# Optimization experiments

Measured on AMD Instinct MI355X. Metric: run time of the kernel, lower is better.

Reference implementation:

```python
import jax, jax.numpy as jnp
import numpy as np

N, E = 50000, 800000
IN_DIM, HID, OUT_DIM = 512, 64, 40


def setup_inputs() -> dict:
    key = jax.random.key(0)
    ks = jax.random.split(key, 7)
    X = jax.random.normal(ks[0], (N, IN_DIM), dtype=jnp.float32)
    edges = jax.random.randint(ks[1], (2, E), 0, N, dtype=jnp.int64)
    # GCNConv weight (glorot) and bias
    W1 = jax.random.normal(ks[2], (IN_DIM, HID), dtype=jnp.float32) / np.sqrt(IN_DIM)
    b1 = jnp.zeros((HID,), dtype=jnp.float32)
    # fc Linear
    Wfc = jax.random.normal(ks[3], (OUT_DIM, HID), dtype=jnp.float32) / np.sqrt(HID)
    bfc = jax.random.normal(ks[4], (OUT_DIM,), dtype=jnp.float32) * 0.01
    return {"X": X, "edges": edges, "W1": W1, "b1": b1, "Wfc": Wfc, "bfc": bfc}


def gcn_conv(x, src, dst, W, b, n):
    # PyG GCNConv: transform, add self-loops, symmetric D^-1/2 A D^-1/2 norm,
    # scatter-add messages at destination, add bias.
    h = x @ W  # [N, HID]
    loop = jnp.arange(n, dtype=src.dtype)
    src = jnp.concatenate([src, loop])
    dst = jnp.concatenate([dst, loop])
    deg = jax.ops.segment_sum(jnp.ones_like(dst, dtype=h.dtype), dst, num_segments=n)
    dinv = jnp.where(deg > 0, jax.lax.rsqrt(deg), 0.0)
    coef = dinv[src] * dinv[dst]  # [E+N]
    msgs = coef[:, None] * h[src]  # gather + scale
    agg = jax.ops.segment_sum(msgs, dst, num_segments=n)  # scatter-add
    return agg + b


def reference(X, edges, W1, b1, Wfc, bfc):
    n = X.shape[0]
    src, dst = edges[0], edges[1]
    h = jax.nn.relu(gcn_conv(X, src, dst, W1, b1, n))  # [N, HID]
    return h @ Wfc.T + bfc  # [N, OUT_DIM]
```

## Files before the change

### kernel.cpp

```cpp
#include <hip/hip_runtime.h>
#include <hip/hip_bf16.h>

typedef unsigned short u16;
typedef __bf16 bf16_8 __attribute__((ext_vector_type(8)));
typedef float f32_4 __attribute__((ext_vector_type(4)));

#define IN_DIM 512
#define HID 64
#define OUT_DIM 40
#define CAP 64
#define CF_BLOCKS 512

__global__ void k_prep(const float* __restrict__ W1, u16* __restrict__ W1t,
                       int* __restrict__ cnt, int n) {
    int i = blockIdx.x * 256 + threadIdx.x;
    if (i < n) cnt[i] = 0;
    if (i < IN_DIM * HID) {
        int k = i / HID, o = i % HID;
        __hip_bfloat16 v = __float2bfloat16(W1[i]);
        W1t[o * IN_DIM + k] = *reinterpret_cast<u16*>(&v);
    }
}

__launch_bounds__(256)
__global__ void k_work(const float* __restrict__ X, const u16* __restrict__ W1t,
                       const int* __restrict__ src, const int* __restrict__ dst,
                       int* cnt, u16* __restrict__ csr, u16* __restrict__ hs,
                       int N, int E, int NT) {
    __shared__ __align__(16) u16 As[2][64 * 40];
    const int t = threadIdx.x;

    if ((int)blockIdx.x >= NT) {
        int tid = ((int)blockIdx.x - NT) * 256 + t;
        int stride = CF_BLOCKS * 256;
        for (int e = tid; e < E; e += stride) {
            int d = dst[e];
            int p = atomicAdd(&cnt[d], 1);
            if (p < CAP) csr[(size_t)d * CAP + p] = (u16)src[e];
        }
        return;
    }

    const int wave = t >> 6;
    const int lane = t & 63;
    const int m = lane & 15;
    const int quad = lane >> 4;
    const int n0 = blockIdx.x * 64;

    f32_4 acc[4];
    #pragma unroll
    for (int c = 0; c < 4; c++) acc[c] = (f32_4){0.f, 0.f, 0.f, 0.f};

    const int r_st = t >> 2;
    const int k_st = (t & 3) * 8;

    int row = n0 + r_st; if (row >= N) row = N - 1;
    const float* xp = X + (size_t)row * IN_DIM + k_st;

    f32_4 x0 = *reinterpret_cast<const f32_4*>(xp);
    f32_4 x1 = *reinterpret_cast<const f32_4*>(xp + 4);

    int buf = 0;
    for (int k0 = 0; k0 < IN_DIM; k0 += 32) {
        u16 xb[8];
        #pragma unroll
        for (int q = 0; q < 4; q++) {
            __hip_bfloat16 c0 = __float2bfloat16(x0[q]);
            __hip_bfloat16 c1 = __float2bfloat16(x1[q]);
            xb[q]     = *reinterpret_cast<u16*>(&c0);
            xb[4 + q] = *reinterpret_cast<u16*>(&c1);
        }
        *reinterpret_cast<uint4*>(&As[buf][r_st * 40 + k_st]) = *reinterpret_cast<uint4*>(xb);
        __syncthreads();

        if (k0 + 32 < IN_DIM) {
            x0 = *reinterpret_cast<const f32_4*>(xp + k0 + 32);
            x1 = *reinterpret_cast<const f32_4*>(xp + k0 + 36);
        }

        bf16_8 a = *reinterpret_cast<const bf16_8*>(&As[buf][(wave * 16 + m) * 40 + quad * 8]);
        #pragma unroll
        for (int c = 0; c < 4; c++) {
            bf16_8 b = *reinterpret_cast<const bf16_8*>(
                W1t + (size_t)(c * 16 + m) * IN_DIM + k0 + quad * 8);
            acc[c] = __builtin_amdgcn_mfma_f32_16x16x32_bf16(a, b, acc[c], 0, 0, 0);
        }
        buf ^= 1;
    }

    const int nbase = n0 + wave * 16 + quad * 4;
    #pragma unroll
    for (int r = 0; r < 4; r++) {
        int n = nbase + r;
        if (n < N) {
            #pragma unroll
            for (int c = 0; c < 4; c++) {
                __hip_bfloat16 hv = __float2bfloat16(acc[c][r]);
                hs[(size_t)n * HID + c * 16 + m] = *reinterpret_cast<u16*>(&hv);
            }
        }
    }
}

__global__ void k_scale(u16* __restrict__ hs, const int* __restrict__ cnt, int N) {
    int i = blockIdx.x * 256 + threadIdx.x;
    int node = i >> 3;
    if (node >= N) return;
    float dv = rsqrtf((float)cnt[node] + 1.0f);
    uint4 v = *reinterpret_cast<uint4*>(hs + (size_t)i * 8);
    uint vv[4] = {v.x, v.y, v.z, v.w};
    u16 o[8];
    #pragma unroll
    for (int q = 0; q < 4; q++) {
        float lo = __uint_as_float(vv[q] << 16) * dv;
        float hi = __uint_as_float(vv[q] & 0xFFFF0000u) * dv;
        __hip_bfloat16 bl_ = __float2bfloat16(lo);
        __hip_bfloat16 bh_ = __float2bfloat16(hi);
        o[2 * q]     = *reinterpret_cast<u16*>(&bl_);
        o[2 * q + 1] = *reinterpret_cast<u16*>(&bh_);
    }
    *reinterpret_cast<uint4*>(hs + (size_t)i * 8) = *reinterpret_cast<uint4*>(o);
}

__device__ __forceinline__ void acc_add(f32_4& a, uint2 v) {
    a[0] += __uint_as_float(v.x << 16);
    a[1] += __uint_as_float(v.x & 0xFFFF0000u);
    a[2] += __uint_as_float(v.y << 16);
    a[3] += __uint_as_float(v.y & 0xFFFF0000u);
}

#define SHP 72

__launch_bounds__(256)
__global__ void k_aggfc(const u16* __restrict__ hs, const u16* __restrict__ csr,
                        const int* __restrict__ cnt, const float* __restrict__ b1,
                        const float* __restrict__ Wfc, const float* __restrict__ bfc,
                        float* __restrict__ out, int N) {
    __shared__ __align__(16) u16 shb[16 * SHP];
    __shared__ __align__(16) u16 wfb[48 * SHP];
    __shared__ float bl[48];
    const int t = threadIdx.x;

    for (int i = t; i < 48 * HID; i += 256) {
        int o = i / HID, k = i % HID;
        float v = (o < OUT_DIM) ? Wfc[o * HID + k] : 0.f;
        __hip_bfloat16 b = __float2bfloat16(v);
        wfb[o * SHP + k] = *reinterpret_cast<u16*>(&b);
    }
    if (t < 48) bl[t] = (t < OUT_DIM) ? bfc[t] : 0.f;

    const int g = t >> 4, l = t & 15;
    const int n = blockIdx.x * 16 + g;

    if (n < N) {
        const uint2* hs2 = reinterpret_cast<const uint2*>(hs);
        f32_4 a0 = (f32_4){0.f, 0.f, 0.f, 0.f};
        f32_4 a1 = a0, a2 = a0, a3 = a0;
        const float dvn = rsqrtf((float)cnt[n] + 1.0f);
        acc_add(a0, hs2[(size_t)n * 16 + l]);
        int deg = cnt[n]; if (deg > CAP) deg = CAP;
        uint2 cv = reinterpret_cast<const uint2*>(csr + (size_t)n * CAP)[l];
        int j = 0;
        for (; j + 7 < deg; j += 8) {
            int base = j >> 2;
            uint w0x = __shfl(cv.x, base, 16);
            uint w0y = __shfl(cv.y, base, 16);
            uint w1x = __shfl(cv.x, base + 1, 16);
            uint w1y = __shfl(cv.y, base + 1, 16);
            int s0 = (int)(w0x & 0xffff), s1 = (int)(w0x >> 16);
            int s2 = (int)(w0y & 0xffff), s3 = (int)(w0y >> 16);
            int s4 = (int)(w1x & 0xffff), s5 = (int)(w1x >> 16);
            int s6 = (int)(w1y & 0xffff), s7 = (int)(w1y >> 16);
            uint2 v0 = hs2[(size_t)s0 * 16 + l];
            uint2 v1 = hs2[(size_t)s1 * 16 + l];
            uint2 v2 = hs2[(size_t)s2 * 16 + l];
            uint2 v3 = hs2[(size_t)s3 * 16 + l];
            uint2 v4 = hs2[(size_t)s4 * 16 + l];
            uint2 v5 = hs2[(size_t)s5 * 16 + l];
            uint2 v6 = hs2[(size_t)s6 * 16 + l];
            uint2 v7 = hs2[(size_t)s7 * 16 + l];
            acc_add(a0, v0); acc_add(a1, v1);
            acc_add(a2, v2); acc_add(a3, v3);
            acc_add(a0, v4); acc_add(a1, v5);
            acc_add(a2, v6); acc_add(a3, v7);
        }
        for (; j < deg; j++) {
            uint w = __shfl(((j >> 1) & 1) ? cv.y : cv.x, j >> 2, 16);
            int s = (int)((w >> ((j & 1) * 16)) & 0xffff);
            acc_add(a0, hs2[(size_t)s * 16 + l]);
        }
        f32_4 acc = (a0 + a1) + (a2 + a3);
        u16 rb[4];
        #pragma unroll
        for (int q = 0; q < 4; q++) {
            float x = dvn * acc[q] + b1[l * 4 + q];
            x = x > 0.f ? x : 0.f;
            __hip_bfloat16 hb = __float2bfloat16(x);
            rb[q] = *reinterpret_cast<u16*>(&hb);
        }
        *reinterpret_cast<uint2*>(&shb[g * SHP + l * 4]) = *reinterpret_cast<uint2*>(rb);
    }
    __syncthreads();

    const int wave = t >> 6;
    const int lane = t & 63;
    const int m = lane & 15;
    const int quad = lane >> 4;
    if (wave < 3) {
        bf16_8 a0 = *reinterpret_cast<const bf16_8*>(&shb[m * SHP + quad * 8]);
        bf16_8 a1 = *reinterpret_cast<const bf16_8*>(&shb[m * SHP + 32 + quad * 8]);
        bf16_8 b0 = *reinterpret_cast<const bf16_8*>(&wfb[(wave * 16 + m) * SHP + quad * 8]);
        bf16_8 b1 = *reinterpret_cast<const bf16_8*>(&wfb[(wave * 16 + m) * SHP + 32 + quad * 8]);
        f32_4 c = (f32_4){0.f, 0.f, 0.f, 0.f};
        c = __builtin_amdgcn_mfma_f32_16x16x32_bf16(a0, b0, c, 0, 0, 0);
        c = __builtin_amdgcn_mfma_f32_16x16x32_bf16(a1, b1, c, 0, 0, 0);
        const int o = wave * 16 + m;
        if (o < OUT_DIM) {
            const int base = blockIdx.x * 16;
            #pragma unroll
            for (int r = 0; r < 4; r++) {
                int node = base + quad * 4 + r;
                if (node < N) out[(size_t)node * OUT_DIM + o] = c[r] + bl[o];
            }
        }
    }
}


extern "C" void kernel_launch(void* const* d_in, const int* in_sizes, int n_in,
                              void* d_out, int out_size, void* d_ws, size_t ws_size,
                              hipStream_t stream) {
    const float* X   = (const float*)d_in[0];
    const int* edges = (const int*)d_in[1];
    const float* W1  = (const float*)d_in[2];
    const float* b1  = (const float*)d_in[3];
    const float* Wfc = (const float*)d_in[4];
    const float* bfc = (const float*)d_in[5];

    const int N = in_sizes[0] / IN_DIM;
    const int E = in_sizes[1] / 2;
    const int* src = edges;
    const int* dst = edges + E;

    char* p = (char*)d_ws;
    auto carve = [&](size_t bytes) -> char* {
        char* r = p;
        p += (bytes + 255) & ~(size_t)255;
        return r;
    };
    u16* W1t = (u16*)carve((size_t)IN_DIM * HID * 2);
    u16* hs  = (u16*)carve((size_t)N * HID * 2);
    int* cnt = (int*)carve((size_t)N * 4);
    u16* csr = (u16*)carve((size_t)N * CAP * 2);

    const int nb = (N + 255) / 256;
    const int NT = (N + 63) / 64;

    k_prep <<<nb, 256, 0, stream>>>(W1, W1t, cnt, N);
    k_work <<<NT + CF_BLOCKS, 256, 0, stream>>>(X, W1t, src, dst, cnt, csr, hs, N, E, NT);
    k_scale<<<(N * 8 + 255) / 256, 256, 0, stream>>>(hs, cnt, N);
    k_aggfc<<<(N + 15) / 16, 256, 0, stream>>>(hs, csr, cnt, b1, Wfc, bfc,
                                               (float*)d_out, N);
}
```

Baseline: 232.1 us.

## Partition CSR build by destination slice and widen gather loop to 16 neighbors

The CSR fill blocks are now grouped into eight destination-range slices. Each block scans a strided share of the edges, unrolled four at a time, and only does atomics for destinations in its own slice, which is meant to localize atomic and csr write traffic. Every edge is now read by eight blocks, which multiplies dst reads. The aggregation loop now issues 16 neighbor gathers per iteration with clamped indices and masked accumulation, replacing the 8-wide loop plus scalar tail. This raises memory-level parallelism but wastes loads on padded slots.

```diff
diff --git a/kernel.cpp b/kernel.cpp
--- a/kernel.cpp
+++ b/kernel.cpp
@@ -31,12 +31,40 @@
     const int t = threadIdx.x;
 
     if ((int)blockIdx.x >= NT) {
-        int tid = ((int)blockIdx.x - NT) * 256 + t;
-        int stride = CF_BLOCKS * 256;
-        for (int e = tid; e < E; e += stride) {
+        const int slice = (int)blockIdx.x & 7;
+        const int rank  = ((int)blockIdx.x - NT) >> 3;
+        const int lo = (int)(((long)slice * N) >> 3);
+        const int hi = (int)(((long)(slice + 1) * N) >> 3);
+        const int stride = 64 * 256;
+        int e = rank * 256 + t;
+        for (; e + 3 * stride < E; e += 4 * stride) {
+            int d0 = dst[e];
+            int d1 = dst[e + stride];
+            int d2 = dst[e + 2 * stride];
+            int d3 = dst[e + 3 * stride];
+            if (d0 >= lo && d0 < hi) {
+                int p = atomicAdd(&cnt[d0], 1);
+                if (p < CAP) csr[(size_t)d0 * CAP + p] = (u16)src[e];
+            }
+            if (d1 >= lo && d1 < hi) {
+                int p = atomicAdd(&cnt[d1], 1);
+                if (p < CAP) csr[(size_t)d1 * CAP + p] = (u16)src[e + stride];
+            }
+            if (d2 >= lo && d2 < hi) {
+                int p = atomicAdd(&cnt[d2], 1);
+                if (p < CAP) csr[(size_t)d2 * CAP + p] = (u16)src[e + 2 * stride];
+            }
+            if (d3 >= lo && d3 < hi) {
+                int p = atomicAdd(&cnt[d3], 1);
+                if (p < CAP) csr[(size_t)d3 * CAP + p] = (u16)src[e + 3 * stride];
+            }
+        }
+        for (; e < E; e += stride) {
             int d = dst[e];
-            int p = atomicAdd(&cnt[d], 1);
-            if (p < CAP) csr[(size_t)d * CAP + p] = (u16)src[e];
+            if (d >= lo && d < hi) {
+                int p = atomicAdd(&cnt[d], 1);
+                if (p < CAP) csr[(size_t)d * CAP + p] = (u16)src[e];
+            }
         }
         return;
     }
@@ -154,42 +182,43 @@
 
     if (n < N) {
         const uint2* hs2 = reinterpret_cast<const uint2*>(hs);
-        f32_4 a0 = (f32_4){0.f, 0.f, 0.f, 0.f};
-        f32_4 a1 = a0, a2 = a0, a3 = a0;
+        f32_4 aa[4];
+        #pragma unroll
+        for (int q = 0; q < 4; q++) aa[q] = (f32_4){0.f, 0.f, 0.f, 0.f};
         const float dvn = rsqrtf((float)cnt[n] + 1.0f);
-        acc_add(a0, hs2[(size_t)n * 16 + l]);
+        acc_add(aa[0], hs2[(size_t)n * 16 + l]);
         int deg = cnt[n]; if (deg > CAP) deg = CAP;
         uint2 cv = reinterpret_cast<const uint2*>(csr + (size_t)n * CAP)[l];
-        int j = 0;
-        for (; j + 7 < deg; j += 8) {
+        const int nn1 = N - 1;
+        for (int j = 0; j < deg; j += 16) {
             int base = j >> 2;
-            uint w0x = __shfl(cv.x, base, 16);
-            uint w0y = __shfl(cv.y, base, 16);
-            uint w1x = __shfl(cv.x, base + 1, 16);
-            uint w1y = __shfl(cv.y, base + 1, 16);
-            int s0 = (int)(w0x & 0xffff), s1 = (int)(w0x >> 16);
-            int s2 = (int)(w0y & 0xffff), s3 = (int)(w0y >> 16);
-            int s4 = (int)(w1x & 0xffff), s5 = (int)(w1x >> 16);
-            int s6 = (int)(w1y & 0xffff), s7 = (int)(w1y >> 16);
-            uint2 v0 = hs2[(size_t)s0 * 16 + l];
-            uint2 v1 = hs2[(size_t)s1 * 16 + l];
-            uint2 v2 = hs2[(size_t)s2 * 16 + l];
-            uint2 v3 = hs2[(size_t)s3 * 16 + l];
-            uint2 v4 = hs2[(size_t)s4 * 16 + l];
-            uint2 v5 = hs2[(size_t)s5 * 16 + l];
-            uint2 v6 = hs2[(size_t)s6 * 16 + l];
-            uint2 v7 = hs2[(size_t)s7 * 16 + l];
-            acc_add(a0, v0); acc_add(a1, v1);
-            acc_add(a2, v2); acc_add(a3, v3);
-            acc_add(a0, v4); acc_add(a1, v5);
-            acc_add(a2, v6); acc_add(a3, v7);
-        }
-        for (; j < deg; j++) {
-            uint w = __shfl(((j >> 1) & 1) ? cv.y : cv.x, j >> 2, 16);
-            int s = (int)((w >> ((j & 1) * 16)) & 0xffff);
-            acc_add(a0, hs2[(size_t)s * 16 + l]);
-        }
-        f32_4 acc = (a0 + a1) + (a2 + a3);
+            uint wx[4], wy[4];
+            #pragma unroll
+            for (int q = 0; q < 4; q++) {
+                wx[q] = __shfl(cv.x, base + q, 16);
+                wy[q] = __shfl(cv.y, base + q, 16);
+            }
+            int s[16];
+            #pragma unroll
+            for (int q = 0; q < 4; q++) {
+                s[4 * q + 0] = (int)(wx[q] & 0xffff);
+                s[4 * q + 1] = (int)(wx[q] >> 16);
+                s[4 * q + 2] = (int)(wy[q] & 0xffff);
+                s[4 * q + 3] = (int)(wy[q] >> 16);
+            }
+            uint2 v[16];
+            #pragma unroll
+            for (int i = 0; i < 16; i++) {
+                int si = s[i] < nn1 ? s[i] : nn1;
+                v[i] = hs2[(size_t)si * 16 + l];
+            }
+            #pragma unroll
+            for (int i = 0; i < 16; i++) {
+                if (j + i >= deg) { v[i].x = 0u; v[i].y = 0u; }
+                acc_add(aa[i & 3], v[i]);
+            }
+        }
+        f32_4 acc = (aa[0] + aa[1]) + (aa[2] + aa[3]);
         u16 rb[4];
         #pragma unroll
         for (int q = 0; q < 4; q++) {
```

Result: slower. 249.4 us (+7.5%).
